# Kernel optimization log

Hardware: AMD Instinct MI355X
Metric: run time of the kernel (lower is better)

Reference implementation:

```python
import jax, jax.numpy as jnp
import numpy as np

N, N_BINS = 100000, 512
BATCH, K = 8192, 16


def setup_inputs() -> dict:
    key = jax.random.key(0)
    k1, k2, k3 = jax.random.split(key, 3)
    outputs = jax.random.uniform(k1, (N, N_BINS), dtype=jnp.float32)
    # y holds (float-encoded) neighbor indices; trunc(y) must index rows of outputs
    y = jax.random.randint(k2, (BATCH, K), 0, N).astype(jnp.float32)
    weights = jax.random.uniform(k3, (BATCH,), dtype=jnp.float32)
    return {"outputs": outputs, "y": y, "weights": weights}


def reference(outputs, y, weights):
    n, n_bins = outputs.shape
    batch_size, k = y.shape
    nns = jnp.trunc(y).astype(jnp.int32)  # (B, k) indices into outputs rows

    # Torch builds add[a,b,c] = outputs[nns[c,a], b] + outputs[c, b] with shape
    # (k, n_bins, batch) then maxes over bins. Equivalent, batch-major layout:
    o_nn = outputs[nns]  # (B, k, n_bins) gather
    add = jnp.max(o_nn + outputs[:batch_size, None, :], axis=-1)  # (B, k)

    booster_weights = jnp.clip((2.0 - jnp.mean(add, axis=1)) / 2.0, 0.5)  # (B,)
    add_mean = jnp.mean(add * weights[:, None])
    diff = jnp.square(2.0 - add_mean)

    target_b = n / n_bins
    b_col = jnp.sum(outputs[:batch_size], axis=0)  # (n_bins,)
    b = jnp.max(b_col) - jnp.min(b_col)

    cost = b / target_b + diff
    return (cost, diff, b / target_b, booster_weights)
```

## Files before the change

### kernel.cpp

```cpp
#include <hip/hip_runtime.h>

#define NBINS 512
#define BDIM 256

__global__ __launch_bounds__(BDIM) void gather_kernel(
        const float* __restrict__ outputs,
        const float* __restrict__ y,
        const float* __restrict__ weights,
        float* __restrict__ out,
        float* __restrict__ wpart,
        int K) {
    __shared__ float s_add[16];

    const int b    = blockIdx.x;
    const int w    = threadIdx.x >> 6;
    const int lane = threadIdx.x & 63;

    const float4* bp = (const float4*)(outputs + (size_t)b * NBINS);
    const float4  b0 = bp[lane];
    const float4  b1 = bp[64 + lane];

    const int kbase = w * 4;
    int nn[4];
    #pragma unroll
    for (int j = 0; j < 4; ++j)
        nn[j] = (int)y[b * K + kbase + j];

    float4 g0[4], g1[4];
    #pragma unroll
    for (int j = 0; j < 4; ++j) {
        const float4* gp = (const float4*)(outputs + (size_t)nn[j] * NBINS);
        g0[j] = gp[lane];
        g1[j] = gp[64 + lane];
    }

    float m[4];
    #pragma unroll
    for (int j = 0; j < 4; ++j) {
        m[j] = fmaxf(fmaxf(fmaxf(g0[j].x + b0.x, g0[j].y + b0.y),
                           fmaxf(g0[j].z + b0.z, g0[j].w + b0.w)),
                     fmaxf(fmaxf(g1[j].x + b1.x, g1[j].y + b1.y),
                           fmaxf(g1[j].z + b1.z, g1[j].w + b1.w)));
    }

    #pragma unroll
    for (int off = 32; off > 0; off >>= 1) {
        #pragma unroll
        for (int j = 0; j < 4; ++j)
            m[j] = fmaxf(m[j], __shfl_down(m[j], off, 64));
    }

    if (lane == 0) {
        s_add[kbase + 0] = m[0];
        s_add[kbase + 1] = m[1];
        s_add[kbase + 2] = m[2];
        s_add[kbase + 3] = m[3];
    }
    __syncthreads();

    if (threadIdx.x == 0) {
        float sum = 0.0f;
        #pragma unroll
        for (int i = 0; i < 16; ++i) sum += s_add[i];
        out[3 + b] = fmaxf(0.5f, (2.0f - sum * (1.0f / 16.0f)) * 0.5f);
        wpart[b] = weights[b] * sum;
    }
}

__global__ __launch_bounds__(NBINS) void colsum_kernel(
        const float* __restrict__ outputs,
        float* __restrict__ part,
        int rows_per_block) {
    const int t = threadIdx.x;
    const size_t r0 = (size_t)blockIdx.x * rows_per_block;
    float local = 0.0f;
    for (int r = 0; r < rows_per_block; ++r)
        local += outputs[(r0 + r) * NBINS + t];
    part[(size_t)blockIdx.x * NBINS + t] = local;
}

__global__ __launch_bounds__(NBINS) void final_kernel(
        const float* __restrict__ part,
        const float* __restrict__ wpart,
        float* __restrict__ out,
        int npart, int B, float inv_count, float inv_target) {
    __shared__ float smax[NBINS];
    __shared__ float smin[NBINS];
    __shared__ float ssum[NBINS];
    const int t = threadIdx.x;

    float v = 0.0f;
    for (int j = 0; j < npart; ++j)
        v += part[(size_t)j * NBINS + t];
    smax[t] = v;
    smin[t] = v;

    float ws = 0.0f;
    for (int i = t; i < B; i += NBINS)
        ws += wpart[i];
    ssum[t] = ws;
    __syncthreads();

    for (int s = NBINS / 2; s > 0; s >>= 1) {
        if (t < s) {
            smax[t] = fmaxf(smax[t], smax[t + s]);
            smin[t] = fminf(smin[t], smin[t + s]);
            ssum[t] += ssum[t + s];
        }
        __syncthreads();
    }
    if (t == 0) {
        float add_mean = ssum[0] * inv_count;
        float d = 2.0f - add_mean;
        float diff = d * d;
        float bn = (smax[0] - smin[0]) * inv_target;
        out[0] = bn + diff;
        out[1] = diff;
        out[2] = bn;
    }
}

extern "C" void kernel_launch(void* const* d_in, const int* in_sizes, int n_in,
                              void* d_out, int out_size, void* d_ws, size_t ws_size,
                              hipStream_t stream) {
    const float* outputs = (const float*)d_in[0];
    const float* y       = (const float*)d_in[1];
    const float* weights = (const float*)d_in[2];
    float* out = (float*)d_out;

    const int B = in_sizes[2];
    const int K = in_sizes[1] / B;
    const int N = in_sizes[0] / NBINS;

    const int COL_BLOCKS = 256;
    const int rows_per_block = B / COL_BLOCKS;

    float* ws      = (float*)d_ws;
    float* wpart   = ws;
    float* colpart = wpart + B;

    gather_kernel<<<B, BDIM, 0, stream>>>(outputs, y, weights, out, wpart, K);
    colsum_kernel<<<COL_BLOCKS, NBINS, 0, stream>>>(outputs, colpart, rows_per_block);
    final_kernel<<<1, NBINS, 0, stream>>>(colpart, wpart, out,
                                          COL_BLOCKS, B,
                                          1.0f / (float)(B * K),
                                          (float)NBINS / (float)N);
}
```

Before: 348.7 us.

## Bucket-sort gather items by neighbor row block before gathering

Adds a counting sort (histogram, scan, scatter) of all (neighbor index, item) pairs by 512-row block of outputs. The gather then walks items in sorted order so nearby rows are fetched together, aiming for better cache locality on the random row gather. Per-item results go to a buffer, and a separate booster kernel reduces them per batch row. The cost is four extra kernel launches, global atomics, and a re-read of the batch row for every item instead of once per block.

```diff
diff --git a/kernel.cpp b/kernel.cpp
--- a/kernel.cpp
+++ b/kernel.cpp
@@ -2,75 +2,126 @@
 
 #define NBINS 512
 #define BDIM 256
+#define MAXHB 1024
+
+
+__global__ void init_hist(int* __restrict__ hist, int hb) {
+    int t = blockIdx.x * blockDim.x + threadIdx.x;
+    if (t < hb) hist[t] = 0;
+}
+
+__global__ __launch_bounds__(BDIM) void count_kernel(
+        const float* __restrict__ y, int* __restrict__ hist,
+        int items, int hb) {
+    __shared__ int lh[MAXHB];
+    for (int i = threadIdx.x; i < hb; i += BDIM) lh[i] = 0;
+    __syncthreads();
+    const int total = gridDim.x * BDIM;
+    for (int i = blockIdx.x * BDIM + threadIdx.x; i < items; i += total) {
+        int nn = (int)y[i];
+        atomicAdd(&lh[nn >> 9], 1);
+    }
+    __syncthreads();
+    for (int i = threadIdx.x; i < hb; i += BDIM)
+        if (lh[i]) atomicAdd(&hist[i], lh[i]);
+}
+
+__global__ __launch_bounds__(MAXHB) void scan_kernel(
+        const int* __restrict__ hist, int* __restrict__ cursor, int hb) {
+    __shared__ int s[MAXHB];
+    const int t = threadIdx.x;
+    int v = (t < hb) ? hist[t] : 0;
+    s[t] = v;
+    __syncthreads();
+    for (int off = 1; off < MAXHB; off <<= 1) {
+        int x = (t >= off) ? s[t - off] : 0;
+        __syncthreads();
+        s[t] += x;
+        __syncthreads();
+    }
+    if (t < hb) cursor[t] = s[t] - v;
+}
+
+__global__ __launch_bounds__(BDIM) void scatter_kernel(
+        const float* __restrict__ y, int* __restrict__ cursor,
+        uint2* __restrict__ itembuf, int items) {
+    const int total = gridDim.x * BDIM;
+    for (int i = blockIdx.x * BDIM + threadIdx.x; i < items; i += total) {
+        int nn = (int)y[i];
+        int pos = atomicAdd(&cursor[nn >> 9], 1);
+        itembuf[pos] = make_uint2((unsigned)nn, (unsigned)i);
+    }
+}
 
 __global__ __launch_bounds__(BDIM) void gather_kernel(
         const float* __restrict__ outputs,
-        const float* __restrict__ y,
+        const uint2* __restrict__ itembuf,
+        float* __restrict__ add,
+        int items, int K) {
+    const int w    = threadIdx.x >> 6;
+    const int lane = threadIdx.x & 63;
+    const int ibase = blockIdx.x * 16 + w * 4;
+
+    uint2 it[4];
+    #pragma unroll
+    for (int j = 0; j < 4; ++j)
+        it[j] = itembuf[min(ibase + j, items - 1)];
+
+    float4 g0[4], g1[4], c0[4], c1[4];
+    #pragma unroll
+    for (int j = 0; j < 4; ++j) {
+        const float4* gp = (const float4*)(outputs + (size_t)it[j].x * NBINS);
+        const unsigned b = it[j].y / (unsigned)K;
+        const float4* bp = (const float4*)(outputs + (size_t)b * NBINS);
+        g0[j] = gp[lane];
+        g1[j] = gp[64 + lane];
+        c0[j] = bp[lane];
+        c1[j] = bp[64 + lane];
+    }
+
+    float m[4];
+    #pragma unroll
+    for (int j = 0; j < 4; ++j) {
+        m[j] = fmaxf(fmaxf(fmaxf(g0[j].x + c0[j].x, g0[j].y + c0[j].y),
+                           fmaxf(g0[j].z + c0[j].z, g0[j].w + c0[j].w)),
+                     fmaxf(fmaxf(g1[j].x + c1[j].x, g1[j].y + c1[j].y),
+                           fmaxf(g1[j].z + c1[j].z, g1[j].w + c1[j].w)));
+    }
+
+    #pragma unroll
+    for (int off = 32; off > 0; off >>= 1) {
+        #pragma unroll
+        for (int j = 0; j < 4; ++j)
+            m[j] = fmaxf(m[j], __shfl_down(m[j], off, 64));
+    }
+
+    if (lane == 0) {
+        #pragma unroll
+        for (int j = 0; j < 4; ++j)
+            if (ibase + j < items) add[it[j].y] = m[j];
+    }
+}
+
+__global__ __launch_bounds__(BDIM) void booster_kernel(
+        const float* __restrict__ add,
         const float* __restrict__ weights,
         float* __restrict__ out,
         float* __restrict__ wpart,
         int K) {
-    __shared__ float s_add[16];
-
-    const int b    = blockIdx.x;
-    const int w    = threadIdx.x >> 6;
-    const int lane = threadIdx.x & 63;
-
-    const float4* bp = (const float4*)(outputs + (size_t)b * NBINS);
-    const float4  b0 = bp[lane];
-    const float4  b1 = bp[64 + lane];
-
-    const int kbase = w * 4;
-    int nn[4];
-    #pragma unroll
-    for (int j = 0; j < 4; ++j)
-        nn[j] = (int)y[b * K + kbase + j];
-
-    float4 g0[4], g1[4];
-    #pragma unroll
-    for (int j = 0; j < 4; ++j) {
-        const float4* gp = (const float4*)(outputs + (size_t)nn[j] * NBINS);
-        g0[j] = gp[lane];
-        g1[j] = gp[64 + lane];
-    }
-
-    float m[4];
-    #pragma unroll
-    for (int j = 0; j < 4; ++j) {
-        m[j] = fmaxf(fmaxf(fmaxf(g0[j].x + b0.x, g0[j].y + b0.y),
-                           fmaxf(g0[j].z + b0.z, g0[j].w + b0.w)),
-                     fmaxf(fmaxf(g1[j].x + b1.x, g1[j].y + b1.y),
-                           fmaxf(g1[j].z + b1.z, g1[j].w + b1.w)));
-    }
-
-    #pragma unroll
-    for (int off = 32; off > 0; off >>= 1) {
-        #pragma unroll
-        for (int j = 0; j < 4; ++j)
-            m[j] = fmaxf(m[j], __shfl_down(m[j], off, 64));
-    }
-
-    if (lane == 0) {
-        s_add[kbase + 0] = m[0];
-        s_add[kbase + 1] = m[1];
-        s_add[kbase + 2] = m[2];
-        s_add[kbase + 3] = m[3];
-    }
-    __syncthreads();
-
-    if (threadIdx.x == 0) {
-        float sum = 0.0f;
-        #pragma unroll
-        for (int i = 0; i < 16; ++i) sum += s_add[i];
-        out[3 + b] = fmaxf(0.5f, (2.0f - sum * (1.0f / 16.0f)) * 0.5f);
-        wpart[b] = weights[b] * sum;
-    }
+    const int b = blockIdx.x * BDIM + threadIdx.x;
+    const float4* ap = (const float4*)(add + (size_t)b * K);
+    float sum = 0.0f;
+    for (int j = 0; j < K / 4; ++j) {
+        float4 a = ap[j];
+        sum += (a.x + a.y) + (a.z + a.w);
+    }
+    out[3 + b] = fmaxf(0.5f, (2.0f - sum / (float)K) * 0.5f);
+    wpart[b] = weights[b] * sum;
 }
 
 __global__ __launch_bounds__(NBINS) void colsum_kernel(
         const float* __restrict__ outputs,
-        float* __restrict__ part,
-        int rows_per_block) {
+        float* __restrict__ part, int rows_per_block) {
     const int t = threadIdx.x;
     const size_t r0 = (size_t)blockIdx.x * rows_per_block;
     float local = 0.0f;
@@ -95,10 +146,10 @@
     smax[t] = v;
     smin[t] = v;
 
-    float ws = 0.0f;
+    float wsum = 0.0f;
     for (int i = t; i < B; i += NBINS)
-        ws += wpart[i];
-    ssum[t] = ws;
+        wsum += wpart[i];
+    ssum[t] = wsum;
     __syncthreads();
 
     for (int s = NBINS / 2; s > 0; s >>= 1) {
@@ -131,16 +182,27 @@
     const int B = in_sizes[2];
     const int K = in_sizes[1] / B;
     const int N = in_sizes[0] / NBINS;
+    const int ITEMS = B * K;
+    const int HB = (N + 511) >> 9;
+
+    char* wsb = (char*)d_ws;
+    int*   hist    = (int*)wsb;
+    int*   cursor  = hist + MAXHB;
+    uint2* itembuf = (uint2*)(wsb + 2 * MAXHB * sizeof(int));
+    float* add     = (float*)(itembuf + ITEMS);
+    float* wpart   = add + ITEMS;
+    float* colpart = wpart + B;
 
     const int COL_BLOCKS = 256;
     const int rows_per_block = B / COL_BLOCKS;
 
-    float* ws      = (float*)d_ws;
-    float* wpart   = ws;
-    float* colpart = wpart + B;
-
-    gather_kernel<<<B, BDIM, 0, stream>>>(outputs, y, weights, out, wpart, K);
+    init_hist<<<(HB + 255) / 256, 256, 0, stream>>>(hist, HB);
+    count_kernel<<<128, BDIM, 0, stream>>>(y, hist, ITEMS, HB);
+    scan_kernel<<<1, MAXHB, 0, stream>>>(hist, cursor, HB);
+    scatter_kernel<<<128, BDIM, 0, stream>>>(y, cursor, itembuf, ITEMS);
+    gather_kernel<<<(ITEMS + 15) / 16, BDIM, 0, stream>>>(outputs, itembuf, add, ITEMS, K);
     colsum_kernel<<<COL_BLOCKS, NBINS, 0, stream>>>(outputs, colpart, rows_per_block);
+    booster_kernel<<<B / BDIM, BDIM, 0, stream>>>(add, weights, out, wpart, K);
     final_kernel<<<1, NBINS, 0, stream>>>(colpart, wpart, out,
                                           COL_BLOCKS, B,
                                           1.0f / (float)(B * K),
```

Measured after the change: 440.7 us. 1.26x slower.

## Drop block sync in gather; move per-row reductions into combined mid kernel

Applied to the files above, without the earlier changes.

The gather kernel no longer reduces its 16 neighbor maxima in shared memory behind a __syncthreads. Each wave writes its four maxima straight to a workspace buffer, and the self-row load is moved after the neighbor gathers. A new mid kernel merges the column-sum work with a pass that sums each row's 16 values to produce the booster weights and weighted partial sums. This removes block-level synchronization and a serial tail from the large gather kernel, at the cost of an extra global round trip of B*K floats.

```diff
diff --git a/kernel.cpp b/kernel.cpp
--- a/kernel.cpp
+++ b/kernel.cpp
@@ -6,19 +6,11 @@
 __global__ __launch_bounds__(BDIM) void gather_kernel(
         const float* __restrict__ outputs,
         const float* __restrict__ y,
-        const float* __restrict__ weights,
-        float* __restrict__ out,
-        float* __restrict__ wpart,
+        float* __restrict__ add,
         int K) {
-    __shared__ float s_add[16];
-
     const int b    = blockIdx.x;
     const int w    = threadIdx.x >> 6;
     const int lane = threadIdx.x & 63;
-
-    const float4* bp = (const float4*)(outputs + (size_t)b * NBINS);
-    const float4  b0 = bp[lane];
-    const float4  b1 = bp[64 + lane];
 
     const int kbase = w * 4;
     int nn[4];
@@ -33,6 +25,10 @@
         g0[j] = gp[lane];
         g1[j] = gp[64 + lane];
     }
+
+    const float4* bp = (const float4*)(outputs + (size_t)b * NBINS);
+    const float4  b0 = bp[lane];
+    const float4  b1 = bp[64 + lane];
 
     float m[4];
     #pragma unroll
@@ -51,36 +47,41 @@
     }
 
     if (lane == 0) {
-        s_add[kbase + 0] = m[0];
-        s_add[kbase + 1] = m[1];
-        s_add[kbase + 2] = m[2];
-        s_add[kbase + 3] = m[3];
+        *((float4*)(add + (size_t)b * K + kbase)) =
+            make_float4(m[0], m[1], m[2], m[3]);
     }
-    __syncthreads();
+}
 
-    if (threadIdx.x == 0) {
+__global__ __launch_bounds__(NBINS) void mid_kernel(
+        const float* __restrict__ outputs,
+        const float* __restrict__ add,
+        const float* __restrict__ weights,
+        float* __restrict__ colpart,
+        float* __restrict__ wpart,
+        float* __restrict__ out,
+        int col_blocks, int rows_per_block, int K) {
+    const int t = threadIdx.x;
+    if (blockIdx.x < (unsigned)col_blocks) {
+        const size_t r0 = (size_t)blockIdx.x * rows_per_block;
+        float local = 0.0f;
+        for (int r = 0; r < rows_per_block; ++r)
+            local += outputs[(r0 + r) * NBINS + t];
+        colpart[(size_t)blockIdx.x * NBINS + t] = local;
+    } else {
+        const int b = (blockIdx.x - col_blocks) * NBINS + t;
+        const float4* ap = (const float4*)(add + (size_t)b * K);
         float sum = 0.0f;
-        #pragma unroll
-        for (int i = 0; i < 16; ++i) sum += s_add[i];
-        out[3 + b] = fmaxf(0.5f, (2.0f - sum * (1.0f / 16.0f)) * 0.5f);
+        for (int j = 0; j < K / 4; ++j) {
+            float4 a = ap[j];
+            sum += (a.x + a.y) + (a.z + a.w);
+        }
+        out[3 + b] = fmaxf(0.5f, (2.0f - sum / (float)K) * 0.5f);
         wpart[b] = weights[b] * sum;
     }
 }
 
-__global__ __launch_bounds__(NBINS) void colsum_kernel(
-        const float* __restrict__ outputs,
-        float* __restrict__ part,
-        int rows_per_block) {
-    const int t = threadIdx.x;
-    const size_t r0 = (size_t)blockIdx.x * rows_per_block;
-    float local = 0.0f;
-    for (int r = 0; r < rows_per_block; ++r)
-        local += outputs[(r0 + r) * NBINS + t];
-    part[(size_t)blockIdx.x * NBINS + t] = local;
-}
-
 __global__ __launch_bounds__(NBINS) void final_kernel(
-        const float* __restrict__ part,
+        const float* __restrict__ colpart,
         const float* __restrict__ wpart,
         float* __restrict__ out,
         int npart, int B, float inv_count, float inv_target) {
@@ -91,14 +92,14 @@
 
     float v = 0.0f;
     for (int j = 0; j < npart; ++j)
-        v += part[(size_t)j * NBINS + t];
+        v += colpart[(size_t)j * NBINS + t];
     smax[t] = v;
     smin[t] = v;
 
-    float ws = 0.0f;
+    float wsum = 0.0f;
     for (int i = t; i < B; i += NBINS)
-        ws += wpart[i];
-    ssum[t] = ws;
+        wsum += wpart[i];
+    ssum[t] = wsum;
     __syncthreads();
 
     for (int s = NBINS / 2; s > 0; s >>= 1) {
@@ -134,13 +135,17 @@
 
     const int COL_BLOCKS = 256;
     const int rows_per_block = B / COL_BLOCKS;
+    const int BOOST_BLOCKS = B / NBINS;
 
     float* ws      = (float*)d_ws;
-    float* wpart   = ws;
+    float* add     = ws;
+    float* wpart   = add + (size_t)B * K;
     float* colpart = wpart + B;
 
-    gather_kernel<<<B, BDIM, 0, stream>>>(outputs, y, weights, out, wpart, K);
-    colsum_kernel<<<COL_BLOCKS, NBINS, 0, stream>>>(outputs, colpart, rows_per_block);
+    gather_kernel<<<B, BDIM, 0, stream>>>(outputs, y, add, K);
+    mid_kernel<<<COL_BLOCKS + BOOST_BLOCKS, NBINS, 0, stream>>>(
+        outputs, add, weights, colpart, wpart, out,
+        COL_BLOCKS, rows_per_block, K);
     final_kernel<<<1, NBINS, 0, stream>>>(colpart, wpart, out,
                                           COL_BLOCKS, B,
                                           1.0f / (float)(B * K),
```

Result: no change. 346.1 us (-0.7%).
